# Optimization experiments

Hardware: AMD Instinct MI355X
Metric: run time of the kernel (lower is better)

Reference implementation:

```python
import jax, jax.numpy as jnp
import numpy as np

L, B, H, P = 2048, 32, 128, 256  # seq len, batch, feature dim, state dim


def setup_inputs() -> dict:
    key = jax.random.key(0)
    ks = jax.random.split(key, 9)
    log_min, log_max = np.log(0.001), np.log(0.1)
    return {
        "input_sequences": jax.random.normal(ks[0], (L, B, H), dtype=jnp.float32),
        # -Lambda.real of a HiPPO block diag is positive; emulate with small positive values
        "log_Lambda_real": jnp.log(0.5 + jax.random.uniform(ks[1], (P,), dtype=jnp.float32)),
        "Lambda_imag": jax.random.normal(ks[2], (P,), dtype=jnp.float32) * 3.0,
        "B_tilde_r": jax.random.normal(ks[3], (P, H), dtype=jnp.float32) * (0.5 / np.sqrt(H)),
        "B_tilde_i": jax.random.normal(ks[4], (P, H), dtype=jnp.float32) * (0.5 / np.sqrt(H)),
        "C_tilde_r": jax.random.normal(ks[5], (H, P), dtype=jnp.float32) * (0.5 / np.sqrt(P)),
        "C_tilde_i": jax.random.normal(ks[6], (H, P), dtype=jnp.float32) * (0.5 / np.sqrt(P)),
        "D": jax.random.normal(ks[7], (H,), dtype=jnp.float32),
        "log_Delta": log_min + (log_max - log_min) * jax.random.uniform(ks[8], (P,), dtype=jnp.float32),
    }


def reference(input_sequences, log_Lambda_real, Lambda_imag, B_tilde_r, B_tilde_i,
              C_tilde_r, C_tilde_i, D, log_Delta):
    l = input_sequences.shape[0]
    u = input_sequences.astype(jnp.complex64)  # (L,B,H)
    lam = (-jnp.exp(log_Lambda_real) + 1j * Lambda_imag).astype(jnp.complex64)  # (P,)
    log_Lambda_bar = lam * jnp.exp(log_Delta).astype(jnp.complex64)  # scale_factor=1.0
    # kernel[t, p] = exp(log_Lambda_bar[p] * (L-1-t))  -> (L,P)
    steps = jnp.arange(l - 1, -1, -1, dtype=jnp.float32).astype(jnp.complex64)
    kernel = jnp.exp(steps[:, None] * log_Lambda_bar[None, :])
    B_tilde = (B_tilde_r + 1j * B_tilde_i).astype(jnp.complex64)  # (P,H)
    B_bar = ((kernel[-2] - 1.0) / lam)[:, None] * B_tilde  # (P,H)
    Bu = jnp.einsum('nm,lbm->lbn', B_bar, u)  # (L,B,P)
    # FFT convolution: flipped kernel is exp(log_Lambda_bar * t)
    kff = jnp.fft.fft(kernel[::-1], n=2 * l, axis=0)[:, None, :]  # (2L,1,P)
    buff = jnp.fft.fft(Bu, n=2 * l, axis=0)  # (2L,B,P)
    o = jnp.fft.ifft(kff * buff, axis=0)[:l]  # (L,B,P)
    xs = jnp.einsum('hn,lbn->lbh', (C_tilde_r + 1j * C_tilde_i).astype(jnp.complex64), o)
    xs = xs + (D * input_sequences).astype(jnp.complex64)
    return jnp.real(xs)
```

## Files before the change

kernel.cpp:

```cpp
#include <hip/hip_runtime.h>
#include <math.h>

#define SL 2048
#define NB 32
#define NH 128
#define NP 256
#define NP2 512

typedef short bf16x8 __attribute__((ext_vector_type(8)));
typedef float f32x4  __attribute__((ext_vector_type(4)));

static __device__ __forceinline__ unsigned short f2bf(float x) {
    unsigned u = __float_as_uint(x);
    return (unsigned short)((u + 0x7fffu + ((u >> 16) & 1u)) >> 16);
}
static __device__ __forceinline__ float bf2f(unsigned short h) {
    return __uint_as_float(((unsigned)h) << 16);
}
static __device__ __forceinline__ void discretize(
    const float* __restrict__ logLr, const float* __restrict__ Lim,
    const float* __restrict__ logDt, int p, float& wr, float& wi)
{
    const float Lr = expf(logLr[p]);
    const float dt = expf(logDt[p]);
    const float ew = expf(-Lr * dt);
    const float ang = Lim[p] * dt;
    wr = ew * cosf(ang); wi = ew * sinf(ang);
}

__global__ __launch_bounds__(256) void k0(
    const float* __restrict__ logLr, const float* __restrict__ Lim,
    const float* __restrict__ logDt,
    const float* __restrict__ Br, const float* __restrict__ Bi,
    const float* __restrict__ Cr, const float* __restrict__ Ci,
    unsigned short* __restrict__ BhatF, unsigned short* __restrict__ ChatF)
{
    const int tid = blockIdx.x * 256 + threadIdx.x;
    const int p = tid >> 7, h = tid & 127;
    float wr, wi; discretize(logLr, Lim, logDt, p, wr, wi);
    const float Lr = expf(logLr[p]), li = Lim[p];
    const float nr = wr - 1.0f, ni = wi;
    const float den = Lr * Lr + li * li;
    const float fr = (-nr * Lr + ni * li) / den;
    const float fi = (-ni * Lr - nr * li) / den;
    const float br = Br[p * NH + h], bi = Bi[p * NH + h];
    BhatF[((size_t)(h >> 5) << 14) + ((2 * p)     << 5) + (h & 31)] = f2bf(fr * br - fi * bi);
    BhatF[((size_t)(h >> 5) << 14) + ((2 * p + 1) << 5) + (h & 31)] = f2bf(fr * bi + fi * br);
    const int col0 = 2 * p, col1 = 2 * p + 1;
    ChatF[((size_t)(col0 >> 5) << 12) + (h << 5) + (col0 & 31)] = f2bf(Cr[h * NP + p]);
    ChatF[((size_t)(col1 >> 5) << 12) + (h << 5) + (col1 & 31)] = f2bf(-Ci[h * NP + p]);
}

__global__ __launch_bounds__(256, 4) void gA(
    const float* __restrict__ u, const unsigned short* __restrict__ BhatF,
    const float* __restrict__ logLr, const float* __restrict__ Lim,
    const float* __restrict__ logDt,
    unsigned short* __restrict__ bu, float2* __restrict__ part)
{
    __shared__ unsigned short us[32][136];
    __shared__ unsigned xs[32 * 129];

    const int m  = blockIdx.x;
    const int ph = blockIdx.y;
    const int b  = blockIdx.z;
    const int tid = threadIdx.x;
    const int w = tid >> 6, lane = tid & 63;
    const int q = lane >> 4, c = lane & 15;
    const int pbase = ph * 256 + w * 64;
    const int l0 = m * 32;

    {
        const int lrow = tid >> 3;
        const int hcol = (tid & 7) * 16;
        const float* up = u + (size_t)(l0 + lrow) * (NB * NH) + b * NH + hcol;
        float4 a = *(const float4*)(up + 0);
        float4 d = *(const float4*)(up + 4);
        float4 e = *(const float4*)(up + 8);
        float4 g = *(const float4*)(up + 12);
        uint4 w0, w1;
        w0.x = (unsigned)f2bf(a.x) | ((unsigned)f2bf(a.y) << 16);
        w0.y = (unsigned)f2bf(a.z) | ((unsigned)f2bf(a.w) << 16);
        w0.z = (unsigned)f2bf(d.x) | ((unsigned)f2bf(d.y) << 16);
        w0.w = (unsigned)f2bf(d.z) | ((unsigned)f2bf(d.w) << 16);
        w1.x = (unsigned)f2bf(e.x) | ((unsigned)f2bf(e.y) << 16);
        w1.y = (unsigned)f2bf(e.z) | ((unsigned)f2bf(e.w) << 16);
        w1.z = (unsigned)f2bf(g.x) | ((unsigned)f2bf(g.y) << 16);
        w1.w = (unsigned)f2bf(g.z) | ((unsigned)f2bf(g.w) << 16);
        *(uint4*)&us[lrow][hcol + 0] = w0;
        *(uint4*)&us[lrow][hcol + 8] = w1;
    }
    __syncthreads();

    f32x4 acc[4][2];
    #pragma unroll
    for (int mt = 0; mt < 4; ++mt)
        #pragma unroll
        for (int nt = 0; nt < 2; ++nt) acc[mt][nt] = (f32x4){0.f, 0.f, 0.f, 0.f};

    #pragma unroll
    for (int kk = 0; kk < 4; ++kk) {
        bf16x8 af[4];
        #pragma unroll
        for (int mt = 0; mt < 4; ++mt)
            af[mt] = *(const bf16x8*)(BhatF + ((size_t)kk << 14)
                                      + ((pbase + 16 * mt + c) << 5) + 8 * q);
        bf16x8 bfr[2];
        #pragma unroll
        for (int nt = 0; nt < 2; ++nt)
            bfr[nt] = *(const bf16x8*)&us[16 * nt + c][kk * 32 + 8 * q];
        #pragma unroll
        for (int mt = 0; mt < 4; ++mt)
            #pragma unroll
            for (int nt = 0; nt < 2; ++nt)
                acc[mt][nt] = __builtin_amdgcn_mfma_f32_16x16x32_bf16(
                    af[mt], bfr[nt], acc[mt][nt], 0, 0, 0);
    }

    #pragma unroll
    for (int mt = 0; mt < 4; ++mt)
        #pragma unroll
        for (int nt = 0; nt < 2; ++nt) {
            const int rw  = 16 * nt + c;
            const int ppl = w * 64 + 16 * mt + 4 * q;
            const int pp  = ph * 256 + ppl;
            ushort4 st;
            st.x = f2bf(acc[mt][nt][0]); st.y = f2bf(acc[mt][nt][1]);
            st.z = f2bf(acc[mt][nt][2]); st.w = f2bf(acc[mt][nt][3]);
            *(ushort4*)(bu + ((size_t)(b * SL + l0 + rw)) * NP2 + pp) = st;
            const int col = (ppl >> 1);
            xs[rw * 129 + col]     = (unsigned)st.x | ((unsigned)st.y << 16);
            xs[rw * 129 + col + 1] = (unsigned)st.z | ((unsigned)st.w << 16);
        }
    __syncthreads();

    if (tid < 128) {
        float wr, wi; discretize(logLr, Lim, logDt, ph * 128 + tid, wr, wi);
        float sr = 0.f, si = 0.f;
        unsigned va[8], vb[8];
        #pragma unroll
        for (int j = 0; j < 8; ++j) va[j] = xs[j * 129 + tid];
        #pragma unroll
        for (int k8 = 0; k8 < 4; ++k8) {
            if (k8 < 3) {
                #pragma unroll
                for (int j = 0; j < 8; ++j) vb[j] = xs[((k8 + 1) * 8 + j) * 129 + tid];
            }
            #pragma unroll
            for (int j = 0; j < 8; ++j) {
                const float xr = bf2f((unsigned short)(va[j] & 0xffffu));
                const float xi = bf2f((unsigned short)(va[j] >> 16));
                const float tr = wr * sr - wi * si + xr;
                const float ti = wr * si + wi * sr + xi;
                sr = tr; si = ti;
            }
            #pragma unroll
            for (int j = 0; j < 8; ++j) va[j] = vb[j];
        }
        part[((size_t)b * 64 + m) * NP + ph * 128 + tid] = make_float2(sr, si);
    }
}

__global__ __launch_bounds__(256) void s2(
    float2* __restrict__ part, const float* __restrict__ logLr,
    const float* __restrict__ Lim, const float* __restrict__ logDt)
{
    const int b = blockIdx.x, p = threadIdx.x;
    float wr, wi; discretize(logLr, Lim, logDt, p, wr, wi);
    float Wr = wr, Wi = wi;
    #pragma unroll
    for (int t = 0; t < 5; ++t) { const float r = Wr * Wr - Wi * Wi; Wi = 2.f * Wr * Wi; Wr = r; }
    const size_t base = (size_t)b * 64 * NP + p;
    float sr = 0.f, si = 0.f;
    float2 va[8], vb[8];
    #pragma unroll
    for (int j = 0; j < 8; ++j) va[j] = part[base + (size_t)j * NP];
    #pragma unroll
    for (int k8 = 0; k8 < 8; ++k8) {
        if (k8 < 7) {
            #pragma unroll
            for (int j = 0; j < 8; ++j)
                vb[j] = part[base + (size_t)((k8 + 1) * 8 + j) * NP];
        }
        #pragma unroll
        for (int j = 0; j < 8; ++j) {
            part[base + (size_t)(k8 * 8 + j) * NP] = make_float2(sr, si);
            const float tr = Wr * sr - Wi * si + va[j].x;
            const float ti = Wr * si + Wi * sr + va[j].y;
            sr = tr; si = ti;
        }
        #pragma unroll
        for (int j = 0; j < 8; ++j) va[j] = vb[j];
    }
}

__global__ __launch_bounds__(256, 4) void gB(
    const unsigned* __restrict__ bu32, const unsigned short* __restrict__ ChatF,
    const float* __restrict__ logLr, const float* __restrict__ Lim,
    const float* __restrict__ logDt, const float2* __restrict__ Ent,
    const float* __restrict__ Dv, const float* __restrict__ u,
    float* __restrict__ out)
{
    __shared__ char   osb[16384];
    __shared__ float2 carr[3 * 128];

    const int m = blockIdx.x, b = blockIdx.y;
    const int tid = threadIdx.x;
    const int w = tid >> 6, lane = tid & 63;
    const int q = lane >> 4, c = lane & 15;
    const int hbase = w * 32;
    const int lbase = m * 32;

    f32x4 acc[2][2];
    #pragma unroll
    for (int mt = 0; mt < 2; ++mt)
        #pragma unroll
        for (int nt = 0; nt < 2; ++nt) acc[mt][nt] = (f32x4){0.f, 0.f, 0.f, 0.f};

    #pragma unroll 1
    for (int half = 0; half < 2; ++half) {
        const int pc0 = half * 128 + lane * 2;

        float wr[2], wi[2];
        #pragma unroll
        for (int e = 0; e < 2; ++e) discretize(logLr, Lim, logDt, pc0 + e, wr[e], wi[e]);

        float Wr[2], Wi[2];
        #pragma unroll
        for (int e = 0; e < 2; ++e) { Wr[e] = wr[e]; Wi[e] = wi[e]; }
        #pragma unroll
        for (int t = 0; t < 3; ++t)
            #pragma unroll
            for (int e = 0; e < 2; ++e) {
                const float r = Wr[e] * Wr[e] - Wi[e] * Wi[e];
                Wi[e] = 2.f * Wr[e] * Wi[e]; Wr[e] = r;
            }

        const unsigned* base = bu32 + ((size_t)(b * SL + m * 32 + w * 8)) * NP
                                    + half * 128 + lane * 2;
        uint2 va[8];
        #pragma unroll
        for (int k = 0; k < 8; ++k) va[k] = *(const uint2*)(base + (size_t)k * NP);

        float sr[2] = {0.f, 0.f}, si[2] = {0.f, 0.f};
        #pragma unroll
        for (int k = 0; k < 8; ++k) {
            unsigned vv[2] = { va[k].x, va[k].y };
            #pragma unroll
            for (int e = 0; e < 2; ++e) {
                const float xr = bf2f((unsigned short)(vv[e] & 0xffffu));
                const float xi = bf2f((unsigned short)(vv[e] >> 16));
                const float tr = wr[e] * sr[e] - wi[e] * si[e] + xr;
                const float ti = wr[e] * si[e] + wi[e] * sr[e] + xi;
                sr[e] = tr; si[e] = ti;
            }
        }
        if (w < 3) {
            #pragma unroll
            for (int e = 0; e < 2; ++e)
                carr[w * 128 + lane * 2 + e] = make_float2(sr[e], si[e]);
        }

        float Er[2], Ei[2];
        #pragma unroll
        for (int e = 0; e < 2; ++e) {
            const float2 E = Ent[((size_t)(b * 64 + m)) * NP + pc0 + e];
            Er[e] = E.x; Ei[e] = E.y;
        }

        __syncthreads();

        #pragma unroll
        for (int j = 0; j < 3; ++j) if (j < w)
            #pragma unroll
            for (int e = 0; e < 2; ++e) {
                const float2 v = carr[j * 128 + lane * 2 + e];
                const float tr = Wr[e] * Er[e] - Wi[e] * Ei[e] + v.x;
                const float ti = Wr[e] * Ei[e] + Wi[e] * Er[e] + v.y;
                Er[e] = tr; Ei[e] = ti;
            }

        #pragma unroll
        for (int e = 0; e < 2; ++e) { sr[e] = Er[e]; si[e] = Ei[e]; }
        #pragma unroll
        for (int k = 0; k < 8; ++k) {
            unsigned vv[2] = { va[k].x, va[k].y };
            unsigned ov[2];
            #pragma unroll
            for (int e = 0; e < 2; ++e) {
                const float xr = bf2f((unsigned short)(vv[e] & 0xffffu));
                const float xi = bf2f((unsigned short)(vv[e] >> 16));
                const float tr = wr[e] * sr[e] - wi[e] * si[e] + xr;
                const float ti = wr[e] * si[e] + wi[e] * sr[e] + xi;
                sr[e] = tr; si[e] = ti;
                ov[e] = (unsigned)f2bf(tr) | ((unsigned)f2bf(ti) << 16);
            }
            const int row = w * 8 + k;
            const unsigned byte = (((unsigned)row << 9) + ((unsigned)lane << 3))
                                  ^ (((unsigned)(row & 7)) << 4);
            uint2 st = { ov[0], ov[1] };
            *(uint2*)(osb + byte) = st;
        }
        __syncthreads();

        #pragma unroll 4
        for (int kl = 0; kl < 8; ++kl) {
            const int kk = half * 8 + kl;
            bf16x8 af[2];
            #pragma unroll
            for (int mt = 0; mt < 2; ++mt)
                af[mt] = *(const bf16x8*)(ChatF + ((size_t)kk << 12)
                                          + ((hbase + (mt << 4) + c) << 5) + (q << 3));
            bf16x8 bfr[2];
            #pragma unroll
            for (int nt = 0; nt < 2; ++nt) {
                const int r = 16 * nt + c;
                const unsigned byte = (((unsigned)r << 9) + ((unsigned)kl << 6)
                                       + ((unsigned)q << 4))
                                      ^ (((unsigned)(c & 7)) << 4);
                bfr[nt] = *(const bf16x8*)(osb + byte);
            }
            #pragma unroll
            for (int mt = 0; mt < 2; ++mt)
                #pragma unroll
                for (int nt = 0; nt < 2; ++nt)
                    acc[mt][nt] = __builtin_amdgcn_mfma_f32_16x16x32_bf16(
                        af[mt], bfr[nt], acc[mt][nt], 0, 0, 0);
        }
        if (half == 0) __syncthreads();
    }

    #pragma unroll
    for (int mt = 0; mt < 2; ++mt) {
        const int h4 = hbase + 16 * mt + 4 * q;
        const float4 dd = *(const float4*)(Dv + h4);
        #pragma unroll
        for (int nt = 0; nt < 2; ++nt) {
            const int l = lbase + 16 * nt + c;
            const size_t off = ((size_t)l * NB + b) * NH + h4;
            const float4 uu = *(const float4*)(u + off);
            float4 ov;
            ov.x = acc[mt][nt][0] + dd.x * uu.x;
            ov.y = acc[mt][nt][1] + dd.y * uu.y;
            ov.z = acc[mt][nt][2] + dd.z * uu.z;
            ov.w = acc[mt][nt][3] + dd.w * uu.w;
            *(float4*)(out + off) = ov;
        }
    }
}

extern "C" void kernel_launch(void* const* d_in, const int* in_sizes, int n_in,
                              void* d_out, int out_size, void* d_ws, size_t ws_size,
                              hipStream_t stream)
{
    const float* u     = (const float*)d_in[0];
    const float* logLr = (const float*)d_in[1];
    const float* Lim   = (const float*)d_in[2];
    const float* Btr   = (const float*)d_in[3];
    const float* Bti   = (const float*)d_in[4];
    const float* Ctr   = (const float*)d_in[5];
    const float* Cti   = (const float*)d_in[6];
    const float* Dv    = (const float*)d_in[7];
    const float* logDt = (const float*)d_in[8];
    float* out = (float*)d_out;

    char* ws = (char*)d_ws;
    unsigned short* bu   = (unsigned short*)ws;
    float2*         part = (float2*)(ws + 67108864);
    unsigned short* Bhat = (unsigned short*)(ws + 71303168);
    unsigned short* Chat = (unsigned short*)(ws + 71434240);

    k0<<<dim3((NP * NH) / 256), 256, 0, stream>>>(logLr, Lim, logDt,
                                                  Btr, Bti, Ctr, Cti, Bhat, Chat);
    gA<<<dim3(SL / 32, 2, NB), 256, 0, stream>>>(u, Bhat, logLr, Lim, logDt, bu, part);
    s2<<<dim3(NB), 256, 0, stream>>>(part, logLr, Lim, logDt);
    gB<<<dim3(SL / 32, NB), 256, 0, stream>>>((const unsigned*)bu, Chat, logLr, Lim,
                                              logDt, part, Dv, u, out);
}
```

Before: 176.8 us.

## Recompute B·u projection in final kernel instead of storing bf16 intermediate

The first GEMM kernel no longer writes the full (B,L,2P) bf16 projected-input tensor to global memory. Instead the final kernel reloads u, recomputes the B-projection with MFMA into shared memory, runs the per-chunk sequential scan seeded by the carried state, and then applies the C projection. This removes a large global write and read of the intermediate, at the cost of doing the input GEMM twice and running a more serialized 32-step scan on only 128 threads per half.

```diff
diff --git a/kernel.cpp b/kernel.cpp
--- a/kernel.cpp
+++ b/kernel.cpp
@@ -54,8 +54,7 @@
 __global__ __launch_bounds__(256, 4) void gA(
     const float* __restrict__ u, const unsigned short* __restrict__ BhatF,
     const float* __restrict__ logLr, const float* __restrict__ Lim,
-    const float* __restrict__ logDt,
-    unsigned short* __restrict__ bu, float2* __restrict__ part)
+    const float* __restrict__ logDt, float2* __restrict__ part)
 {
     __shared__ unsigned short us[32][136];
     __shared__ unsigned xs[32 * 129];
@@ -122,11 +121,9 @@
         for (int nt = 0; nt < 2; ++nt) {
             const int rw  = 16 * nt + c;
             const int ppl = w * 64 + 16 * mt + 4 * q;
-            const int pp  = ph * 256 + ppl;
             ushort4 st;
             st.x = f2bf(acc[mt][nt][0]); st.y = f2bf(acc[mt][nt][1]);
             st.z = f2bf(acc[mt][nt][2]); st.w = f2bf(acc[mt][nt][3]);
-            *(ushort4*)(bu + ((size_t)(b * SL + l0 + rw)) * NP2 + pp) = st;
             const int col = (ppl >> 1);
             xs[rw * 129 + col]     = (unsigned)st.x | ((unsigned)st.y << 16);
             xs[rw * 129 + col + 1] = (unsigned)st.z | ((unsigned)st.w << 16);
@@ -193,139 +190,152 @@
     }
 }
 
-__global__ __launch_bounds__(256, 4) void gB(
-    const unsigned* __restrict__ bu32, const unsigned short* __restrict__ ChatF,
+__global__ __launch_bounds__(256, 4) void gF(
+    const float* __restrict__ u, const unsigned short* __restrict__ BhatF,
+    const unsigned short* __restrict__ ChatF,
     const float* __restrict__ logLr, const float* __restrict__ Lim,
     const float* __restrict__ logDt, const float2* __restrict__ Ent,
-    const float* __restrict__ Dv, const float* __restrict__ u,
-    float* __restrict__ out)
-{
-    __shared__ char   osb[16384];
-    __shared__ float2 carr[3 * 128];
+    const float* __restrict__ Dv, float* __restrict__ out)
+{
+    __shared__ unsigned short us[32][136];
+    __shared__ char osb[16384];
 
     const int m = blockIdx.x, b = blockIdx.y;
     const int tid = threadIdx.x;
     const int w = tid >> 6, lane = tid & 63;
     const int q = lane >> 4, c = lane & 15;
     const int hbase = w * 32;
-    const int lbase = m * 32;
-
-    f32x4 acc[2][2];
+    const int l0 = m * 32;
+
+    {
+        const int lrow = tid >> 3;
+        const int hcol = (tid & 7) * 16;
+        const float* up = u + (size_t)(l0 + lrow) * (NB * NH) + b * NH + hcol;
+        float4 a = *(const float4*)(up + 0);
+        float4 d = *(const float4*)(up + 4);
+        float4 e = *(const float4*)(up + 8);
+        float4 g = *(const float4*)(up + 12);
+        uint4 w0, w1;
+        w0.x = (unsigned)f2bf(a.x) | ((unsigned)f2bf(a.y) << 16);
+        w0.y = (unsigned)f2bf(a.z) | ((unsigned)f2bf(a.w) << 16);
+        w0.z = (unsigned)f2bf(d.x) | ((unsigned)f2bf(d.y) << 16);
+        w0.w = (unsigned)f2bf(d.z) | ((unsigned)f2bf(d.w) << 16);
+        w1.x = (unsigned)f2bf(e.x) | ((unsigned)f2bf(e.y) << 16);
+        w1.y = (unsigned)f2bf(e.z) | ((unsigned)f2bf(e.w) << 16);
+        w1.z = (unsigned)f2bf(g.x) | ((unsigned)f2bf(g.y) << 16);
+        w1.w = (unsigned)f2bf(g.z) | ((unsigned)f2bf(g.w) << 16);
+        *(uint4*)&us[lrow][hcol + 0] = w0;
+        *(uint4*)&us[lrow][hcol + 8] = w1;
+    }
+    __syncthreads();
+
+    f32x4 acc2[2][2];
     #pragma unroll
     for (int mt = 0; mt < 2; ++mt)
         #pragma unroll
-        for (int nt = 0; nt < 2; ++nt) acc[mt][nt] = (f32x4){0.f, 0.f, 0.f, 0.f};
+        for (int nt = 0; nt < 2; ++nt) acc2[mt][nt] = (f32x4){0.f, 0.f, 0.f, 0.f};
 
     #pragma unroll 1
     for (int half = 0; half < 2; ++half) {
-        const int pc0 = half * 128 + lane * 2;
-
-        float wr[2], wi[2];
-        #pragma unroll
-        for (int e = 0; e < 2; ++e) discretize(logLr, Lim, logDt, pc0 + e, wr[e], wi[e]);
-
-        float Wr[2], Wi[2];
-        #pragma unroll
-        for (int e = 0; e < 2; ++e) { Wr[e] = wr[e]; Wi[e] = wi[e]; }
-        #pragma unroll
-        for (int t = 0; t < 3; ++t)
-            #pragma unroll
-            for (int e = 0; e < 2; ++e) {
-                const float r = Wr[e] * Wr[e] - Wi[e] * Wi[e];
-                Wi[e] = 2.f * Wr[e] * Wi[e]; Wr[e] = r;
-            }
-
-        const unsigned* base = bu32 + ((size_t)(b * SL + m * 32 + w * 8)) * NP
-                                    + half * 128 + lane * 2;
-        uint2 va[8];
-        #pragma unroll
-        for (int k = 0; k < 8; ++k) va[k] = *(const uint2*)(base + (size_t)k * NP);
-
-        float sr[2] = {0.f, 0.f}, si[2] = {0.f, 0.f};
-        #pragma unroll
-        for (int k = 0; k < 8; ++k) {
-            unsigned vv[2] = { va[k].x, va[k].y };
-            #pragma unroll
-            for (int e = 0; e < 2; ++e) {
-                const float xr = bf2f((unsigned short)(vv[e] & 0xffffu));
-                const float xi = bf2f((unsigned short)(vv[e] >> 16));
-                const float tr = wr[e] * sr[e] - wi[e] * si[e] + xr;
-                const float ti = wr[e] * si[e] + wi[e] * sr[e] + xi;
-                sr[e] = tr; si[e] = ti;
-            }
-        }
-        if (w < 3) {
-            #pragma unroll
-            for (int e = 0; e < 2; ++e)
-                carr[w * 128 + lane * 2 + e] = make_float2(sr[e], si[e]);
-        }
-
-        float Er[2], Ei[2];
-        #pragma unroll
-        for (int e = 0; e < 2; ++e) {
-            const float2 E = Ent[((size_t)(b * 64 + m)) * NP + pc0 + e];
-            Er[e] = E.x; Ei[e] = E.y;
-        }
-
-        __syncthreads();
-
-        #pragma unroll
-        for (int j = 0; j < 3; ++j) if (j < w)
-            #pragma unroll
-            for (int e = 0; e < 2; ++e) {
-                const float2 v = carr[j * 128 + lane * 2 + e];
-                const float tr = Wr[e] * Er[e] - Wi[e] * Ei[e] + v.x;
-                const float ti = Wr[e] * Ei[e] + Wi[e] * Er[e] + v.y;
-                Er[e] = tr; Ei[e] = ti;
-            }
-
-        #pragma unroll
-        for (int e = 0; e < 2; ++e) { sr[e] = Er[e]; si[e] = Ei[e]; }
-        #pragma unroll
-        for (int k = 0; k < 8; ++k) {
-            unsigned vv[2] = { va[k].x, va[k].y };
-            unsigned ov[2];
-            #pragma unroll
-            for (int e = 0; e < 2; ++e) {
-                const float xr = bf2f((unsigned short)(vv[e] & 0xffffu));
-                const float xi = bf2f((unsigned short)(vv[e] >> 16));
-                const float tr = wr[e] * sr[e] - wi[e] * si[e] + xr;
-                const float ti = wr[e] * si[e] + wi[e] * sr[e] + xi;
-                sr[e] = tr; si[e] = ti;
-                ov[e] = (unsigned)f2bf(tr) | ((unsigned)f2bf(ti) << 16);
-            }
-            const int row = w * 8 + k;
-            const unsigned byte = (((unsigned)row << 9) + ((unsigned)lane << 3))
-                                  ^ (((unsigned)(row & 7)) << 4);
-            uint2 st = { ov[0], ov[1] };
-            *(uint2*)(osb + byte) = st;
-        }
-        __syncthreads();
-
-        #pragma unroll 4
-        for (int kl = 0; kl < 8; ++kl) {
-            const int kk = half * 8 + kl;
-            bf16x8 af[2];
-            #pragma unroll
-            for (int mt = 0; mt < 2; ++mt)
-                af[mt] = *(const bf16x8*)(ChatF + ((size_t)kk << 12)
-                                          + ((hbase + (mt << 4) + c) << 5) + (q << 3));
+        const int pbase = half * 256 + w * 64;
+        f32x4 acc[4][2];
+        #pragma unroll
+        for (int mt = 0; mt < 4; ++mt)
+            #pragma unroll
+            for (int nt = 0; nt < 2; ++nt) acc[mt][nt] = (f32x4){0.f, 0.f, 0.f, 0.f};
+        #pragma unroll
+        for (int kk = 0; kk < 4; ++kk) {
+            bf16x8 af[4];
+            #pragma unroll
+            for (int mt = 0; mt < 4; ++mt)
+                af[mt] = *(const bf16x8*)(BhatF + ((size_t)kk << 14)
+                                          + ((pbase + 16 * mt + c) << 5) + 8 * q);
             bf16x8 bfr[2];
             #pragma unroll
-            for (int nt = 0; nt < 2; ++nt) {
-                const int r = 16 * nt + c;
-                const unsigned byte = (((unsigned)r << 9) + ((unsigned)kl << 6)
-                                       + ((unsigned)q << 4))
-                                      ^ (((unsigned)(c & 7)) << 4);
-                bfr[nt] = *(const bf16x8*)(osb + byte);
-            }
-            #pragma unroll
-            for (int mt = 0; mt < 2; ++mt)
+            for (int nt = 0; nt < 2; ++nt)
+                bfr[nt] = *(const bf16x8*)&us[16 * nt + c][kk * 32 + 8 * q];
+            #pragma unroll
+            for (int mt = 0; mt < 4; ++mt)
                 #pragma unroll
                 for (int nt = 0; nt < 2; ++nt)
                     acc[mt][nt] = __builtin_amdgcn_mfma_f32_16x16x32_bf16(
                         af[mt], bfr[nt], acc[mt][nt], 0, 0, 0);
         }
+
+        #pragma unroll
+        for (int mt = 0; mt < 4; ++mt)
+            #pragma unroll
+            for (int nt = 0; nt < 2; ++nt) {
+                const int row  = 16 * nt + c;
+                const int col2 = w * 32 + 8 * mt + 2 * q;
+                ushort4 st;
+                st.x = f2bf(acc[mt][nt][0]); st.y = f2bf(acc[mt][nt][1]);
+                st.z = f2bf(acc[mt][nt][2]); st.w = f2bf(acc[mt][nt][3]);
+                const unsigned byte = (((unsigned)row << 9)
+                                       + (((unsigned)col2 << 2)
+                                          ^ (((unsigned)(row & 7)) << 4)));
+                uint2 st2 = { (unsigned)st.x | ((unsigned)st.y << 16),
+                              (unsigned)st.z | ((unsigned)st.w << 16) };
+                *(uint2*)(osb + byte) = st2;
+            }
+        __syncthreads();
+
+        if (tid < 128) {
+            const int p = half * 128 + tid;
+            float wr, wi; discretize(logLr, Lim, logDt, p, wr, wi);
+            const float2 E = Ent[((size_t)(b * 64 + m)) * NP + p];
+            float sr = E.x, si = E.y;
+            unsigned va[32];
+            #pragma unroll
+            for (int j = 0; j < 32; ++j) {
+                const unsigned byte = (((unsigned)j << 9)
+                                       + (((unsigned)tid << 2)
+                                          ^ (((unsigned)(j & 7)) << 4)));
+                va[j] = *(const unsigned*)(osb + byte);
+            }
+            #pragma unroll
+            for (int j = 0; j < 32; ++j) {
+                const float xr = bf2f((unsigned short)(va[j] & 0xffffu));
+                const float xi = bf2f((unsigned short)(va[j] >> 16));
+                const float tr = wr * sr - wi * si + xr;
+                const float ti = wr * si + wi * sr + xi;
+                sr = tr; si = ti;
+                va[j] = (unsigned)f2bf(tr) | ((unsigned)f2bf(ti) << 16);
+            }
+            #pragma unroll
+            for (int j = 0; j < 32; ++j) {
+                const unsigned byte = (((unsigned)j << 9)
+                                       + (((unsigned)tid << 2)
+                                          ^ (((unsigned)(j & 7)) << 4)));
+                *(unsigned*)(osb + byte) = va[j];
+            }
+        }
+        __syncthreads();
+
+        #pragma unroll 4
+        for (int kl = 0; kl < 8; ++kl) {
+            const int kk = half * 8 + kl;
+            bf16x8 af2[2];
+            #pragma unroll
+            for (int mt = 0; mt < 2; ++mt)
+                af2[mt] = *(const bf16x8*)(ChatF + ((size_t)kk << 12)
+                                           + ((hbase + (mt << 4) + c) << 5) + (q << 3));
+            bf16x8 bfr2[2];
+            #pragma unroll
+            for (int nt = 0; nt < 2; ++nt) {
+                const int r = 16 * nt + c;
+                const unsigned byte = ((((unsigned)r << 9) + ((unsigned)kl << 6)
+                                        + ((unsigned)q << 4))
+                                       ^ (((unsigned)(c & 7)) << 4));
+                bfr2[nt] = *(const bf16x8*)(osb + byte);
+            }
+            #pragma unroll
+            for (int mt = 0; mt < 2; ++mt)
+                #pragma unroll
+                for (int nt = 0; nt < 2; ++nt)
+                    acc2[mt][nt] = __builtin_amdgcn_mfma_f32_16x16x32_bf16(
+                        af2[mt], bfr2[nt], acc2[mt][nt], 0, 0, 0);
+        }
         if (half == 0) __syncthreads();
     }
 
@@ -335,14 +345,14 @@
         const float4 dd = *(const float4*)(Dv + h4);
         #pragma unroll
         for (int nt = 0; nt < 2; ++nt) {
-            const int l = lbase + 16 * nt + c;
+            const int l = l0 + 16 * nt + c;
             const size_t off = ((size_t)l * NB + b) * NH + h4;
             const float4 uu = *(const float4*)(u + off);
             float4 ov;
-            ov.x = acc[mt][nt][0] + dd.x * uu.x;
-            ov.y = acc[mt][nt][1] + dd.y * uu.y;
-            ov.z = acc[mt][nt][2] + dd.z * uu.z;
-            ov.w = acc[mt][nt][3] + dd.w * uu.w;
+            ov.x = acc2[mt][nt][0] + dd.x * uu.x;
+            ov.y = acc2[mt][nt][1] + dd.y * uu.y;
+            ov.z = acc2[mt][nt][2] + dd.z * uu.z;
+            ov.w = acc2[mt][nt][3] + dd.w * uu.w;
             *(float4*)(out + off) = ov;
         }
     }
@@ -364,15 +374,14 @@
     float* out = (float*)d_out;
 
     char* ws = (char*)d_ws;
-    unsigned short* bu   = (unsigned short*)ws;
-    float2*         part = (float2*)(ws + 67108864);
-    unsigned short* Bhat = (unsigned short*)(ws + 71303168);
-    unsigned short* Chat = (unsigned short*)(ws + 71434240);
+    float2*         part = (float2*)ws;
+    unsigned short* Bhat = (unsigned short*)(ws + 4194304);
+    unsigned short* Chat = (unsigned short*)(ws + 4325376);
 
     k0<<<dim3((NP * NH) / 256), 256, 0, stream>>>(logLr, Lim, logDt,
                                                   Btr, Bti, Ctr, Cti, Bhat, Chat);
-    gA<<<dim3(SL / 32, 2, NB), 256, 0, stream>>>(u, Bhat, logLr, Lim, logDt, bu, part);
+    gA<<<dim3(SL / 32, 2, NB), 256, 0, stream>>>(u, Bhat, logLr, Lim, logDt, part);
     s2<<<dim3(NB), 256, 0, stream>>>(part, logLr, Lim, logDt);
-    gB<<<dim3(SL / 32, NB), 256, 0, stream>>>((const unsigned*)bu, Chat, logLr, Lim,
-                                              logDt, part, Dv, u, out);
-}
+    gF<<<dim3(SL / 32, NB), 256, 0, stream>>>(u, Bhat, Chat, logLr, Lim, logDt,
+                                              part, Dv, out);
+}
```

After: 168.4 us. -4.8%, faster.
